# Performance work log

Hardware: AMD Instinct MI355X
Metric: run time of the kernel (lower is better)

The kernel has to match this reference:

```python
import jax, jax.numpy as jnp
import numpy as np

N = 100000
E = 1600000
D_IN = 128
D_HID = 128
D_OUT = 64


def setup_inputs() -> dict:
    key = jax.random.key(0)
    ks = jax.random.split(key, 12)
    x = jax.random.normal(ks[0], (N, D_IN), dtype=jnp.float32)
    src = jax.random.randint(ks[1], (E,), 0, N, dtype=jnp.int32)
    dst = jax.random.randint(ks[2], (E,), 0, N, dtype=jnp.int32)
    def lin(k, din, dout):
        s = 1.0 / np.sqrt(din)
        return jax.random.uniform(k, (din, dout), jnp.float32, -s, s)
    return {
        "x": x, "src": src, "dst": dst,
        "Ws0": lin(ks[3], D_IN, D_HID), "Wn0": lin(ks[4], D_IN, D_HID), "b0": jnp.zeros((D_HID,), jnp.float32),
        "Ws1": lin(ks[5], D_HID, D_HID), "Wn1": lin(ks[6], D_HID, D_HID), "b1": jnp.zeros((D_HID,), jnp.float32),
        "Ws2": lin(ks[7], D_HID, D_OUT), "Wn2": lin(ks[8], D_HID, D_OUT), "b2": jnp.zeros((D_OUT,), jnp.float32),
    }


def _sage_conv(h, src, dst, Ws, Wn, b):
    # mean aggregation of neighbor (src) features onto dst nodes
    deg = jax.ops.segment_sum(jnp.ones((src.shape[0],), h.dtype), dst, num_segments=N)
    agg = jax.ops.segment_sum(h[src], dst, num_segments=N)  # [N, d_in]
    mean = agg / jnp.maximum(deg, 1.0)[:, None]
    return h @ Ws + mean @ Wn + b


def reference(x, src, dst, Ws0, Wn0, b0, Ws1, Wn1, b1, Ws2, Wn2, b2):
    h = _sage_conv(x, src, dst, Ws0, Wn0, b0)
    h = jax.nn.relu(h)  # dropout is identity in eval mode
    h = _sage_conv(h, src, dst, Ws1, Wn1, b1)
    h = jax.nn.relu(h)
    h = _sage_conv(h, src, dst, Ws2, Wn2, b2)
    return h
```

## Files before the change

### kernel.cpp

```cpp
#include <hip/hip_runtime.h>

#define NN 100000
#define NE 1600000
#define DF 128
#define TS 136
#define NCB 391
#define NWA 256
#define SZA 6250
#define NH (NCB * NWA)
#define CAPB 6144

typedef unsigned int uint32;
typedef unsigned short u16;
typedef _Float16 f16;
typedef f16 f16x8 __attribute__((ext_vector_type(8)));
typedef f16 f16x2 __attribute__((ext_vector_type(2)));
typedef float f32x4 __attribute__((ext_vector_type(4)));

__device__ __forceinline__ float2 up2(uint32 u) {
    union { uint32 u; f16x2 h; } v; v.u = u;
    return make_float2((float)v.h.x, (float)v.h.y);
}
__device__ __forceinline__ uint32 pk2(float a, float b) {
    union { f16x2 h; uint32 u; } v;
    v.h.x = (f16)a; v.h.y = (f16)b;
    return v.u;
}
__device__ __forceinline__ u16 f2h(float a) {
    union { f16 h; u16 u; } v; v.h = (f16)a; return v.u;
}
__device__ __forceinline__ float h2f(u16 a) {
    union { u16 u; f16 h; } v; v.u = a; return (float)v.h;
}


__global__ __launch_bounds__(256) void histA(const int* __restrict__ dst,
                                             int* __restrict__ H) {
    __shared__ int lh[NCB];
    int w = blockIdx.x, t = threadIdx.x;
    for (int i = t; i < NCB; i += 256) lh[i] = 0;
    __syncthreads();
    int e0 = w * SZA, e1 = min(e0 + SZA, NE);
    for (int e = e0 + t; e < e1; e += 256) atomicAdd(&lh[dst[e] >> 8], 1);
    __syncthreads();
    for (int i = t; i < NCB; i += 256) H[i * NWA + w] = lh[i];
}

__global__ __launch_bounds__(256) void sumCB(const int* __restrict__ H,
                                             int* __restrict__ CBT) {
    __shared__ int sm[256];
    int cb = blockIdx.x, t = threadIdx.x;
    sm[t] = H[cb * NWA + t];
    __syncthreads();
    for (int off = 128; off > 0; off >>= 1) {
        if (t < off) sm[t] += sm[t + off];
        __syncthreads();
    }
    if (t == 0) CBT[cb] = sm[0];
}

__global__ __launch_bounds__(512) void scanCB(const int* __restrict__ CBT,
                                              int* __restrict__ CBO,
                                              int* __restrict__ O,
                                              int* __restrict__ rowptr) {
    __shared__ int sm[512];
    int t = threadIdx.x;
    int v = (t < NCB) ? CBT[t] : 0;
    sm[t] = v;
    __syncthreads();
    for (int off = 1; off < 512; off <<= 1) {
        int x = (t >= off) ? sm[t - off] : 0;
        __syncthreads();
        sm[t] += x;
        __syncthreads();
    }
    if (t < NCB) CBO[t] = sm[t] - v;
    if (t == NCB - 1) {
        O[NH] = sm[t];
        rowptr[NN] = sm[t];
    }
}

__global__ __launch_bounds__(256) void scanW(const int* __restrict__ H,
                                             const int* __restrict__ CBO,
                                             int* __restrict__ O) {
    __shared__ int sm[256];
    int cb = blockIdx.x, t = threadIdx.x;
    int v = H[cb * NWA + t];
    sm[t] = v;
    __syncthreads();
    for (int off = 1; off < 256; off <<= 1) {
        int x = (t >= off) ? sm[t - off] : 0;
        __syncthreads();
        sm[t] += x;
        __syncthreads();
    }
    O[cb * NWA + t] = CBO[cb] + sm[t] - v;
}

__global__ __launch_bounds__(1024) void passA(const int* __restrict__ src,
                                              const int* __restrict__ dst,
                                              const int* __restrict__ O,
                                              uint32* __restrict__ ebuf) {
    __shared__ int cur[NCB];
    int w = blockIdx.x, t = threadIdx.x;
    for (int i = t; i < NCB; i += 1024) cur[i] = O[i * NWA + w];
    __syncthreads();
    int e0 = w * SZA, e1 = min(e0 + SZA, NE);
    for (int e = e0 + t; e < e1; e += 1024) {
        int d = dst[e];
        int cb = d >> 8;
        int p = atomicAdd(&cur[cb], 1);
        ebuf[p] = ((uint32)src[e] << 8) | (uint32)(d & 255);
    }
}

__global__ __launch_bounds__(256) void passB(const uint32* __restrict__ ebuf,
                                             const int* __restrict__ O,
                                             int* __restrict__ rowptr,
                                             int* __restrict__ col) {
    __shared__ int hist[256], start[256], cur[256];
    __shared__ int seg[CAPB];
    int cb = blockIdx.x, t = threadIdx.x;
    int base = O[cb * NWA], end = O[(cb + 1) * NWA];
    int m = end - base;
    hist[t] = 0;
    __syncthreads();
    for (int i = t; i < m; i += 256) atomicAdd(&hist[ebuf[base + i] & 255], 1);
    __syncthreads();
    int v = hist[t];
    cur[t] = v;
    __syncthreads();
    for (int off = 1; off < 256; off <<= 1) {
        int x = (t >= off) ? cur[t - off] : 0;
        __syncthreads();
        cur[t] += x;
        __syncthreads();
    }
    start[t] = cur[t] - v;
    __syncthreads();
    int node = cb * 256 + t;
    if (node < NN) rowptr[node] = base + start[t];
    cur[t] = start[t];
    __syncthreads();
    if (m <= CAPB) {
        for (int i = t; i < m; i += 256) {
            uint32 u = ebuf[base + i];
            int p = atomicAdd(&cur[u & 255], 1);
            seg[p] = (int)(u >> 8);
        }
        __syncthreads();
        for (int i = t; i < m; i += 256) col[base + i] = seg[i];
    } else {
        for (int i = t; i < m; i += 256) {
            uint32 u = ebuf[base + i];
            int p = atomicAdd(&cur[u & 255], 1);
            col[base + p] = (int)(u >> 8);
        }
    }
}

__global__ void prep_all(const float* __restrict__ Ws0, const float* __restrict__ Wn0,
                         const float* __restrict__ Ws1, const float* __restrict__ Wn1,
                         const float* __restrict__ Ws2, const float* __restrict__ Wn2,
                         u16* __restrict__ WB) {
    int t = blockIdx.x * 256 + threadIdx.x;
    if (t < 65536) {
        int m = t >> 14;
        int local = t & 16383;
        int k = local >> 7, n = local & 127;
        const float* W = (m == 0) ? Ws0 : (m == 1) ? Wn0 : (m == 2) ? Ws1 : Wn1;
        WB[m * 16384 + n * 128 + k] = f2h(W[k * 128 + n]);
    } else {
        int local = t - 65536;
        int half = local >> 13;
        int idx = local & 8191;
        int k = idx >> 6, n = idx & 63;
        const float* W = half ? Wn2 : Ws2;
        WB[4 * 16384 + (n + half * 64) * 128 + k] = f2h(W[k * 64 + n]);
    }
}

__global__ void cvt_f16(const float* __restrict__ x, uint2* __restrict__ xh) {
    int t = blockIdx.x * 256 + threadIdx.x;
    if (t < NN * DF / 4) {
        float4 v = ((const float4*)x)[t];
        uint2 o;
        o.x = pk2(v.x, v.y);
        o.y = pk2(v.z, v.w);
        xh[t] = o;
    }
}

__global__ __launch_bounds__(256) void gather_f16(const u16* __restrict__ hb,
                                                  const int* __restrict__ rowptr,
                                                  const int* __restrict__ col,
                                                  u16* __restrict__ mean) {
    int bid = blockIdx.x;
    int panel = bid & 1;
    int node = (bid >> 1) * 32 + (threadIdx.x >> 3);
    int g = threadIdx.x & 7;
    const u16* hp = hb + panel * 64 + g * 8;
    int s = rowptr[node], e = rowptr[node + 1];
    float acc[8];
#pragma unroll
    for (int i = 0; i < 8; ++i) acc[i] = 0.f;
    int j = s;
    for (; j + 3 < e; j += 4) {
        int n0 = col[j], n1 = col[j + 1], n2 = col[j + 2], n3 = col[j + 3];
        f16x8 v0 = *(const f16x8*)(hp + (size_t)n0 * DF);
        f16x8 v1 = *(const f16x8*)(hp + (size_t)n1 * DF);
        f16x8 v2 = *(const f16x8*)(hp + (size_t)n2 * DF);
        f16x8 v3 = *(const f16x8*)(hp + (size_t)n3 * DF);
        f16x8 s01 = v0 + v1;
        f16x8 s23 = v2 + v3;
        f16x8 sv = s01 + s23;
#pragma unroll
        for (int i = 0; i < 8; ++i) acc[i] += (float)sv[i];
    }
    for (; j < e; ++j) {
        f16x8 v = *(const f16x8*)(hp + (size_t)col[j] * DF);
#pragma unroll
        for (int i = 0; i < 8; ++i) acc[i] += (float)v[i];
    }
    float invd = 1.f / fmaxf((float)(e - s), 1.f);
    union { f16x8 h; uint4 u; } o;
#pragma unroll
    for (int i = 0; i < 8; ++i) o.h[i] = (f16)(acc[i] * invd);
    *(uint4*)(mean + (size_t)node * DF + panel * 64 + g * 8) = o.u;
}

__global__ __launch_bounds__(256) void gather_add_f16(const u16* __restrict__ gb,
                                                      const int* __restrict__ rowptr,
                                                      const int* __restrict__ col,
                                                      float* __restrict__ out) {
    int node = blockIdx.x * 32 + (threadIdx.x >> 3);
    int g = threadIdx.x & 7;
    int s = rowptr[node], e = rowptr[node + 1];
    float acc[8];
#pragma unroll
    for (int i = 0; i < 8; ++i) acc[i] = 0.f;
    int j = s;
    for (; j + 3 < e; j += 4) {
        int n0 = col[j], n1 = col[j + 1], n2 = col[j + 2], n3 = col[j + 3];
        f16x8 v0 = *(const f16x8*)(gb + (size_t)n0 * 64 + g * 8);
        f16x8 v1 = *(const f16x8*)(gb + (size_t)n1 * 64 + g * 8);
        f16x8 v2 = *(const f16x8*)(gb + (size_t)n2 * 64 + g * 8);
        f16x8 v3 = *(const f16x8*)(gb + (size_t)n3 * 64 + g * 8);
        f16x8 s01 = v0 + v1;
        f16x8 s23 = v2 + v3;
        f16x8 sv = s01 + s23;
#pragma unroll
        for (int i = 0; i < 8; ++i) acc[i] += (float)sv[i];
    }
    for (; j < e; ++j) {
        f16x8 v = *(const f16x8*)(gb + (size_t)col[j] * 64 + g * 8);
#pragma unroll
        for (int i = 0; i < 8; ++i) acc[i] += (float)v[i];
    }
    float invd = 1.f / fmaxf((float)(e - s), 1.f);
    float4* op = (float4*)(out + (size_t)node * 64 + g * 8);
    float4 a = op[0], b = op[1];
    a.x += acc[0] * invd; a.y += acc[1] * invd;
    a.z += acc[2] * invd; a.w += acc[3] * invd;
    b.x += acc[4] * invd; b.y += acc[5] * invd;
    b.z += acc[6] * invd; b.w += acc[7] * invd;
    op[0] = a; op[1] = b;
}

__device__ __forceinline__ void stage_a(u16* sm, const u16* g, int row0, int tid) {
#pragma unroll
    for (int i = 0; i < 8; ++i) {
        int idx = i * 256 + tid;
        int r = idx >> 4, c = (idx & 15) * 8;
        uint4 v = make_uint4(0, 0, 0, 0);
        int gr = row0 + r;
        if (gr < NN) v = *(const uint4*)(g + (size_t)gr * DF + c);
        *(uint4*)(sm + r * TS + c) = v;
    }
}

__device__ __forceinline__ void stage_w(u16* sm, const u16* wt, int nbase, int tid) {
#pragma unroll
    for (int i = 0; i < 4; ++i) {
        int idx = i * 256 + tid;
        int r = idx >> 4, c = (idx & 15) * 8;
        *(uint4*)(sm + r * TS + c) = *(const uint4*)(wt + (size_t)(nbase + r) * 128 + c);
    }
}

__device__ __forceinline__ f16x8 frag(const u16* sm, int row, int lane, int kc) {
    return *(const f16x8*)(sm + (row + (lane & 15)) * TS + kc * 32 + (lane >> 4) * 8);
}

__device__ __forceinline__ void mfma4(const u16* As, const u16* Bs, int wrow, int lane,
                                      f32x4 acc[2][8], int ab) {
    f16x8 a[2][4];
#pragma unroll
    for (int rt = 0; rt < 2; ++rt)
#pragma unroll
        for (int kc = 0; kc < 4; ++kc) a[rt][kc] = frag(As, wrow + rt * 16, lane, kc);
#pragma unroll
    for (int n = 0; n < 4; ++n) {
#pragma unroll
        for (int kc = 0; kc < 4; ++kc) {
            f16x8 b = frag(Bs, n * 16, lane, kc);
            acc[0][ab + n] = __builtin_amdgcn_mfma_f32_16x16x32_f16(a[0][kc], b, acc[0][ab + n], 0, 0, 0);
            acc[1][ab + n] = __builtin_amdgcn_mfma_f32_16x16x32_f16(a[1][kc], b, acc[1][ab + n], 0, 0, 0);
        }
    }
}

#define SW(WT, NB) { __syncthreads(); stage_w(Bs, WT, NB, tid); __syncthreads(); }

__global__ __launch_bounds__(256) void gemm_sage_f16(
    const u16* H, const u16* M,
    const u16* __restrict__ Ws, const u16* __restrict__ Wn,
    const float* __restrict__ bias, u16* OutH) {
    __shared__ u16 As[128 * TS];
    __shared__ u16 Bs[64 * TS];
    const int tid = threadIdx.x;
    const int lane = tid & 63;
    const int wrow = (tid >> 6) * 32;
    const int row0 = blockIdx.x * 128;

    f32x4 acc[2][8];
#pragma unroll
    for (int rt = 0; rt < 2; ++rt)
#pragma unroll
        for (int n = 0; n < 8; ++n) acc[rt][n] = {0.f, 0.f, 0.f, 0.f};

    stage_a(As, H, row0, tid);
    stage_w(Bs, Ws, 0, tid);
    __syncthreads();
    mfma4(As, Bs, wrow, lane, acc, 0);
    SW(Ws, 64); mfma4(As, Bs, wrow, lane, acc, 4);
    __syncthreads();
    stage_a(As, M, row0, tid);
    stage_w(Bs, Wn, 0, tid);
    __syncthreads();
    mfma4(As, Bs, wrow, lane, acc, 0);
    SW(Wn, 64); mfma4(As, Bs, wrow, lane, acc, 4);

    const int cit = lane & 15;
    const int rq = (lane >> 4) * 4;
#pragma unroll
    for (int rt = 0; rt < 2; ++rt)
#pragma unroll
        for (int n = 0; n < 8; ++n) {
            float bv = bias[n * 16 + cit];
            f32x4 v = acc[rt][n];
#pragma unroll
            for (int r = 0; r < 4; ++r) {
                int gr = row0 + wrow + rt * 16 + rq + r;
                if (gr < NN) {
                    float o = fmaxf(v[r] + bv, 0.f);
                    OutH[(size_t)gr * DF + n * 16 + cit] = f2h(o);
                }
            }
        }
}

__global__ __launch_bounds__(256) void gemm_l2_f16(
    const u16* __restrict__ H, const u16* __restrict__ W2,
    const float* __restrict__ b2, float* __restrict__ out, u16* __restrict__ g2) {
    __shared__ u16 As[128 * TS];
    __shared__ u16 Bs[64 * TS];
    const int tid = threadIdx.x;
    const int lane = tid & 63;
    const int wrow = (tid >> 6) * 32;
    const int row0 = blockIdx.x * 128;

    f32x4 acc[2][8];
#pragma unroll
    for (int rt = 0; rt < 2; ++rt)
#pragma unroll
        for (int n = 0; n < 8; ++n) acc[rt][n] = {0.f, 0.f, 0.f, 0.f};

    stage_a(As, H, row0, tid);
    stage_w(Bs, W2, 0, tid);
    __syncthreads();
    mfma4(As, Bs, wrow, lane, acc, 0);
    SW(W2, 64); mfma4(As, Bs, wrow, lane, acc, 4);

    const int cit = lane & 15;
    const int rq = (lane >> 4) * 4;
#pragma unroll
    for (int rt = 0; rt < 2; ++rt)
#pragma unroll
        for (int n = 0; n < 8; ++n) {
            f32x4 v = acc[rt][n];
            float bv = (n < 4) ? b2[n * 16 + cit] : 0.f;
#pragma unroll
            for (int r = 0; r < 4; ++r) {
                int gr = row0 + wrow + rt * 16 + rq + r;
                if (gr < NN) {
                    if (n < 4) out[(size_t)gr * 64 + n * 16 + cit] = v[r] + bv;
                    else g2[(size_t)gr * 64 + (n - 4) * 16 + cit] = f2h(v[r]);
                }
            }
        }
}

extern "C" void kernel_launch(void* const* d_in, const int* in_sizes, int n_in,
                              void* d_out, int out_size, void* d_ws, size_t ws_size,
                              hipStream_t stream) {
    const float* x   = (const float*)d_in[0];
    const int*   src = (const int*)d_in[1];
    const int*   dst = (const int*)d_in[2];
    const float* Ws0 = (const float*)d_in[3];
    const float* Wn0 = (const float*)d_in[4];
    const float* b0  = (const float*)d_in[5];
    const float* Ws1 = (const float*)d_in[6];
    const float* Wn1 = (const float*)d_in[7];
    const float* b1  = (const float*)d_in[8];
    const float* Ws2 = (const float*)d_in[9];
    const float* Wn2 = (const float*)d_in[10];
    const float* b2  = (const float*)d_in[11];
    float* out = (float*)d_out;

    int* H       = (int*)d_ws;
    int* O       = H + NH;
    int* CBT     = O + 100352;
    int* CBO     = CBT + 512;
    int* rowptr  = CBO + 512;
    int* col     = rowptr + 100352;
    uint32* ebuf = (uint32*)(col + NE);
    u16* WB      = (u16*)(ebuf + NE);
    u16* W0s = WB, *W0n = WB + 16384, *W1s = WB + 2 * 16384, *W1n = WB + 3 * 16384;
    u16* W2  = WB + 4 * 16384;
    u16* P1 = WB + 5 * 16384;
    u16* P3 = P1 + (size_t)NN * DF;

    const int gB = (NN + 127) / 128;

    histA<<<NWA, 256, 0, stream>>>(dst, H);
    sumCB<<<NCB, 256, 0, stream>>>(H, CBT);
    scanCB<<<1, 512, 0, stream>>>(CBT, CBO, O, rowptr);
    scanW<<<NCB, 256, 0, stream>>>(H, CBO, O);
    passA<<<NWA, 1024, 0, stream>>>(src, dst, O, ebuf);
    passB<<<NCB, 256, 0, stream>>>(ebuf, O, rowptr, col);

    prep_all<<<320, 256, 0, stream>>>(Ws0, Wn0, Ws1, Wn1, Ws2, Wn2, WB);

    cvt_f16<<<NN * DF / 4 / 256, 256, 0, stream>>>(x, (uint2*)P1);

    gather_f16<<<(NN / 32) * 2, 256, 0, stream>>>(P1, rowptr, col, P3);
    gemm_sage_f16<<<gB, 256, 0, stream>>>(P1, P3, W0s, W0n, b0, P1);

    gather_f16<<<(NN / 32) * 2, 256, 0, stream>>>(P1, rowptr, col, P3);
    gemm_sage_f16<<<gB, 256, 0, stream>>>(P1, P3, W1s, W1n, b1, P1);

    gemm_l2_f16<<<gB, 256, 0, stream>>>(P1, W2, b2, out, P3);
    gather_add_f16<<<NN / 32, 256, 0, stream>>>(P3, rowptr, col, out);
}
```

Before: 388.7 us.

## Assign gather panels per XCC via atomic work queues for L2 locality

The two-panel feature gather now pulls work from per-panel atomic chunk counters instead of using a fixed blockIdx mapping. Each block reads its XCC id and takes chunks from the panel queue tied to that die, falling back to the other panel once that queue is drained. The aim is for each XCC's private L2 to cache only half of the feature columns, raising the hit rate on random neighbor rows. The cost is one global atomic per block plus a shared-memory broadcast, and some imbalance if the XCC split is uneven.

```diff
diff --git a/kernel.cpp b/kernel.cpp
--- a/kernel.cpp
+++ b/kernel.cpp
@@ -9,6 +9,7 @@
 #define SZA 6250
 #define NH (NCB * NWA)
 #define CAPB 6144
+#define NCHUNK 3125
 
 typedef unsigned int uint32;
 typedef unsigned short u16;
@@ -33,6 +34,12 @@
     union { u16 u; f16 h; } v; v.u = a; return (float)v.h;
 }
 
+__device__ __forceinline__ int xcc_id() {
+    int x;
+    asm volatile("s_getreg_b32 %0, hwreg(HW_REG_XCC_ID)" : "=s"(x));
+    return x & 7;
+}
+
 
 __global__ __launch_bounds__(256) void histA(const int* __restrict__ dst,
                                              int* __restrict__ H) {
@@ -62,9 +69,11 @@
 __global__ __launch_bounds__(512) void scanCB(const int* __restrict__ CBT,
                                               int* __restrict__ CBO,
                                               int* __restrict__ O,
-                                              int* __restrict__ rowptr) {
+                                              int* __restrict__ rowptr,
+                                              int* __restrict__ QC) {
     __shared__ int sm[512];
     int t = threadIdx.x;
+    if (t == 0) { QC[0] = 0; QC[32] = 0; QC[64] = 0; QC[96] = 0; }
     int v = (t < NCB) ? CBT[t] : 0;
     sm[t] = v;
     __syncthreads();
@@ -195,10 +204,21 @@
 __global__ __launch_bounds__(256) void gather_f16(const u16* __restrict__ hb,
                                                   const int* __restrict__ rowptr,
                                                   const int* __restrict__ col,
-                                                  u16* __restrict__ mean) {
-    int bid = blockIdx.x;
-    int panel = bid & 1;
-    int node = (bid >> 1) * 32 + (threadIdx.x >> 3);
+                                                  u16* __restrict__ mean,
+                                                  int* __restrict__ q) {
+    __shared__ int sh_chunk, sh_panel;
+    if (threadIdx.x == 0) {
+        int p = xcc_id() & 1;
+        int i = atomicAdd(&q[p * 32], 1);
+        if (i >= NCHUNK) { p ^= 1; i = atomicAdd(&q[p * 32], 1); }
+        sh_chunk = (i < NCHUNK) ? i : -1;
+        sh_panel = p;
+    }
+    __syncthreads();
+    int chunk = sh_chunk;
+    if (chunk < 0) return;
+    int panel = sh_panel;
+    int node = chunk * 32 + (threadIdx.x >> 3);
     int g = threadIdx.x & 7;
     const u16* hp = hb + panel * 64 + g * 8;
     int s = rowptr[node], e = rowptr[node + 1];
@@ -431,12 +451,13 @@
     u16* W2  = WB + 4 * 16384;
     u16* P1 = WB + 5 * 16384;
     u16* P3 = P1 + (size_t)NN * DF;
+    int* QC = CBT + 400;
 
     const int gB = (NN + 127) / 128;
 
     histA<<<NWA, 256, 0, stream>>>(dst, H);
     sumCB<<<NCB, 256, 0, stream>>>(H, CBT);
-    scanCB<<<1, 512, 0, stream>>>(CBT, CBO, O, rowptr);
+    scanCB<<<1, 512, 0, stream>>>(CBT, CBO, O, rowptr, QC);
     scanW<<<NCB, 256, 0, stream>>>(H, CBO, O);
     passA<<<NWA, 1024, 0, stream>>>(src, dst, O, ebuf);
     passB<<<NCB, 256, 0, stream>>>(ebuf, O, rowptr, col);
@@ -445,10 +466,10 @@
 
     cvt_f16<<<NN * DF / 4 / 256, 256, 0, stream>>>(x, (uint2*)P1);
 
-    gather_f16<<<(NN / 32) * 2, 256, 0, stream>>>(P1, rowptr, col, P3);
+    gather_f16<<<NCHUNK * 2, 256, 0, stream>>>(P1, rowptr, col, P3, QC);
     gemm_sage_f16<<<gB, 256, 0, stream>>>(P1, P3, W0s, W0n, b0, P1);
 
-    gather_f16<<<(NN / 32) * 2, 256, 0, stream>>>(P1, rowptr, col, P3);
+    gather_f16<<<NCHUNK * 2, 256, 0, stream>>>(P1, rowptr, col, P3, QC + 64);
     gemm_sage_f16<<<gB, 256, 0, stream>>>(P1, P3, W1s, W1n, b1, P1);
 
     gemm_l2_f16<<<gB, 256, 0, stream>>>(P1, W2, b2, out, P3);
```

Result: slower. 420.3 us (+8.1%).
